# Performance work log

Measured on AMD Instinct MI355X. Metric: run time of the kernel, lower is better.

## Reference

```python
import jax, jax.numpy as jnp
import numpy as np

N_USERS, N_ITEMS, DIM, LAYERS, NNZ = 50000, 50000, 128, 2, 1600000
N = N_USERS + N_ITEMS


def setup_inputs() -> dict:
    key = jax.random.key(0)
    ks = jax.random.split(key, 8)
    adj_row = jax.random.randint(ks[0], (NNZ,), 0, N, dtype=jnp.int32)
    adj_col = jax.random.randint(ks[1], (NNZ,), 0, N, dtype=jnp.int32)
    # normalized-adjacency-like small positive values (~1/avg_degree)
    adj_vals = jax.random.uniform(ks[2], (NNZ,), dtype=jnp.float32) * 0.0625
    emb = jax.random.normal(ks[3], (N, DIM), dtype=jnp.float32) * 0.1  # xavier-ish
    W1_w = jax.random.normal(ks[4], (LAYERS, DIM, DIM), dtype=jnp.float32) * (1.0 / np.sqrt(DIM))
    W1_b = jnp.zeros((LAYERS, DIM), dtype=jnp.float32)
    W2_w = jax.random.normal(ks[5], (LAYERS, DIM, DIM), dtype=jnp.float32) * (1.0 / np.sqrt(DIM))
    W2_b = jnp.zeros((LAYERS, DIM), dtype=jnp.float32)
    return {"adj_row": adj_row, "adj_col": adj_col, "adj_vals": adj_vals,
            "emb": emb, "W1_w": W1_w, "W1_b": W1_b, "W2_w": W2_w, "W2_b": W2_b}


def reference(adj_row, adj_col, adj_vals, emb, W1_w, W1_b, W2_w, W2_b):
    n = emb.shape[0]
    x = emb
    embs = [x]
    for k in range(W1_w.shape[0]):
        # SpMM: side = norm_adj @ x  (COO gather + segment-sum)
        side = jax.ops.segment_sum(adj_vals[:, None] * x[adj_col], adj_row, num_segments=n)
        # two dense transforms (torch Linear: y = x @ W.T + b), fused add + leaky_relu
        x = jax.nn.leaky_relu((side + x) @ W1_w[k].T + W1_b[k]
                              + (side * x) @ W2_w[k].T + W2_b[k],
                              negative_slope=0.01)
        # dropout is identity in eval mode; L2-normalize rows (F.normalize eps=1e-12)
        x = x / jnp.maximum(jnp.linalg.norm(x, axis=1, keepdims=True), 1e-12)
        embs.append(x)
    return jnp.concatenate(embs, axis=1)  # [N, dim*(layers+1)]
```

## Files before the change

### kernel.cpp

```cpp
#include <hip/hip_runtime.h>
#include <stdint.h>

#define N_NODES 100000
#define NPAD    100032
#define DIM 128
#define NNZ_E 1600000
#define SCAN_TILE 2048
#define N_TILES ((N_NODES + SCAN_TILE - 1) / SCAN_TILE)

typedef float f32x4  __attribute__((ext_vector_type(4)));
typedef short bf16x8 __attribute__((ext_vector_type(8)));

union B8 { uint4 q; unsigned u[4]; bf16x8 v; };

__device__ __forceinline__ unsigned short f2bs(float f) {
    unsigned u = __builtin_bit_cast(unsigned, f);
    u = (u + 0x7fffu + ((u >> 16) & 1u)) >> 16;
    return (unsigned short)u;
}
__device__ __forceinline__ unsigned pk2(float a, float b) {
    return (unsigned)f2bs(a) | ((unsigned)f2bs(b) << 16);
}
#define UNPK(u32, flo, fhi) { flo = __builtin_bit_cast(float, (unsigned)((u32) << 16)); \
                              fhi = __builtin_bit_cast(float, (unsigned)((u32) & 0xffff0000u)); }

__global__ __launch_bounds__(256) void copy_emb_kernel(
    const float* __restrict__ emb, float* __restrict__ out,
    unsigned* __restrict__ xbuf)
{
    int tid = blockIdx.x * 256 + threadIdx.x;
    int n = tid >> 5, c = tid & 31;
    float4 v = ((const float4*)emb)[tid];
    *((float4*)(out + (size_t)n * 384) + c) = v;
    ((uint2*)xbuf)[(size_t)n * 32 + c] = make_uint2(pk2(v.x, v.y), pk2(v.z, v.w));
}

__global__ __launch_bounds__(256) void wconv_kernel(
    const float* __restrict__ W1, const float* __restrict__ W2,
    unsigned* __restrict__ w1b, unsigned* __restrict__ w2b)
{
    int tid = blockIdx.x * 256 + threadIdx.x;
    float4 a = ((const float4*)W1)[tid];
    float4 b = ((const float4*)W2)[tid];
    ((uint2*)w1b)[tid] = make_uint2(pk2(a.x, a.y), pk2(a.z, a.w));
    ((uint2*)w2b)[tid] = make_uint2(pk2(b.x, b.y), pk2(b.z, b.w));
}

__global__ __launch_bounds__(256) void hist_kernel(
    const int* __restrict__ rows, int* __restrict__ cnt)
{
    int e = blockIdx.x * 256 + threadIdx.x;
    atomicAdd(&cnt[rows[e]], 1);
}

__global__ __launch_bounds__(256) void scan_pass_a(
    const int* __restrict__ cnt, int* __restrict__ tile_sums)
{
    __shared__ int sdata[256];
    int base = blockIdx.x * SCAN_TILE + threadIdx.x * 8;
    int s = 0;
    #pragma unroll
    for (int q = 0; q < 8; ++q) {
        int i = base + q;
        s += (i < N_NODES) ? cnt[i] : 0;
    }
    sdata[threadIdx.x] = s;
    __syncthreads();
    for (int off = 128; off >= 1; off >>= 1) {
        if (threadIdx.x < off) sdata[threadIdx.x] += sdata[threadIdx.x + off];
        __syncthreads();
    }
    if (threadIdx.x == 0) tile_sums[blockIdx.x] = sdata[0];
}

__global__ void scan_pass_b(int* __restrict__ tile_sums)
{
    if (threadIdx.x == 0 && blockIdx.x == 0) {
        int acc = 0;
        for (int i = 0; i < N_TILES; ++i) {
            int t = tile_sums[i]; tile_sums[i] = acc; acc += t;
        }
    }
}

__global__ __launch_bounds__(256) void scan_pass_c(
    const int* __restrict__ cnt, const int* __restrict__ tile_offs,
    int* __restrict__ row_ptr)
{
    __shared__ int spart[256];
    int t = threadIdx.x;
    int base = blockIdx.x * SCAN_TILE + t * 8;
    int loc[8];
    int s = 0;
    #pragma unroll
    for (int q = 0; q < 8; ++q) {
        int i = base + q;
        int c = (i < N_NODES) ? cnt[i] : 0;
        loc[q] = s; s += c;
    }
    spart[t] = s;
    __syncthreads();
    for (int off = 1; off < 256; off <<= 1) {
        int v = (t >= off) ? spart[t - off] : 0;
        __syncthreads();
        spart[t] += v;
        __syncthreads();
    }
    int exoff = tile_offs[blockIdx.x] + spart[t] - s;
    #pragma unroll
    for (int q = 0; q < 8; ++q) {
        int i = base + q;
        if (i <= N_NODES) row_ptr[i] = exoff + loc[q];
    }
}

__global__ __launch_bounds__(256) void scatter_kernel(
    const int* __restrict__ rows, const int* __restrict__ cols,
    const float* __restrict__ vals, const int* __restrict__ row_ptr,
    int* __restrict__ fill, int2* __restrict__ edges)
{
    int e = blockIdx.x * 256 + threadIdx.x;
    int r = rows[e];
    int pos = row_ptr[r] + atomicAdd(&fill[r], 1);
    edges[pos] = make_int2(cols[e], __float_as_int(vals[e]));
}

__global__ __launch_bounds__(256) void spmm_gather_bf16(
    const int* __restrict__ row_ptr, const int2* __restrict__ edges,
    const unsigned* __restrict__ xb, unsigned* __restrict__ sideb)
{
    int row  = blockIdx.x * 4 + (threadIdx.x >> 6);
    int lane = threadIdx.x & 63;
    int beg = row_ptr[row], end = row_ptr[row + 1];
    float ax = 0.f, ay = 0.f;
    int i = beg;
    for (; i + 3 < end; i += 4) {
        int2 e0 = edges[i], e1 = edges[i + 1], e2 = edges[i + 2], e3 = edges[i + 3];
        unsigned u0 = xb[(size_t)e0.x * 64 + lane];
        unsigned u1 = xb[(size_t)e1.x * 64 + lane];
        unsigned u2 = xb[(size_t)e2.x * 64 + lane];
        unsigned u3 = xb[(size_t)e3.x * 64 + lane];
        float v0 = __int_as_float(e0.y), v1 = __int_as_float(e1.y);
        float v2 = __int_as_float(e2.y), v3 = __int_as_float(e3.y);
        float lo, hi;
        UNPK(u0, lo, hi); ax += v0 * lo; ay += v0 * hi;
        UNPK(u1, lo, hi); ax += v1 * lo; ay += v1 * hi;
        UNPK(u2, lo, hi); ax += v2 * lo; ay += v2 * hi;
        UNPK(u3, lo, hi); ax += v3 * lo; ay += v3 * hi;
    }
    for (; i < end; ++i) {
        int2 e = edges[i];
        unsigned u = xb[(size_t)e.x * 64 + lane];
        float v = __int_as_float(e.y), lo, hi;
        UNPK(u, lo, hi); ax += v * lo; ay += v * hi;
    }
    sideb[(size_t)row * 64 + lane] = pk2(ax, ay);
}

__global__ __launch_bounds__(256) void dense_mfma_kernel(
    const unsigned* __restrict__ sideb, unsigned* __restrict__ xbuf,
    const unsigned* __restrict__ w1b, const unsigned* __restrict__ w2b,
    const float* __restrict__ b1, const float* __restrict__ b2,
    float* __restrict__ out, int outoff, int write_x)
{
    __shared__ float sPart[256];
    const int t = threadIdx.x;
    const int wave = t >> 6, lane = t & 63;
    const int q = lane >> 4, r = lane & 15;
    const int colbase = wave * 32;

    bf16x8 Wf[2][2][4];
    {
        const uint4* w1p = (const uint4*)w1b;
        const uint4* w2p = (const uint4*)w2b;
        #pragma unroll
        for (int nt = 0; nt < 2; ++nt) {
            int j = colbase + nt * 16 + r;
            #pragma unroll
            for (int kk = 0; kk < 4; ++kk) {
                B8 a, b;
                a.q = w1p[j * 16 + kk * 4 + q];
                b.q = w2p[j * 16 + kk * 4 + q];
                Wf[0][nt][kk] = a.v;
                Wf[1][nt][kk] = b.v;
            }
        }
    }
    const float bias0 = b1[colbase + r]      + b2[colbase + r];
    const float bias1 = b1[colbase + 16 + r] + b2[colbase + 16 + r];

    const int base = blockIdx.x * 64;
    f32x4 acc[4][2];
    #pragma unroll
    for (int mt = 0; mt < 4; ++mt) {
        acc[mt][0] = (f32x4){0.f, 0.f, 0.f, 0.f};
        acc[mt][1] = (f32x4){0.f, 0.f, 0.f, 0.f};
    }

    #pragma unroll
    for (int mt = 0; mt < 4; ++mt) {
        const size_t node = (size_t)(base + mt * 16 + r);
        const uint4* sp = (const uint4*)sideb + node * 16 + q;
        const uint4* xp = (const uint4*)xbuf  + node * 16 + q;
        #pragma unroll
        for (int kk = 0; kk < 4; ++kk) {
            uint4 sv = sp[kk * 4];
            uint4 xv = xp[kk * 4];
            float s0,s1,s2,s3,s4,s5,s6,s7;
            float x0,x1,x2,x3,x4,x5,x6,x7;
            UNPK(sv.x, s0, s1); UNPK(sv.y, s2, s3);
            UNPK(sv.z, s4, s5); UNPK(sv.w, s6, s7);
            UNPK(xv.x, x0, x1); UNPK(xv.y, x2, x3);
            UNPK(xv.z, x4, x5); UNPK(xv.w, x6, x7);
            B8 a1, a2;
            a1.u[0] = pk2(s0 + x0, s1 + x1);
            a1.u[1] = pk2(s2 + x2, s3 + x3);
            a1.u[2] = pk2(s4 + x4, s5 + x5);
            a1.u[3] = pk2(s6 + x6, s7 + x7);
            a2.u[0] = pk2(s0 * x0, s1 * x1);
            a2.u[1] = pk2(s2 * x2, s3 * x3);
            a2.u[2] = pk2(s4 * x4, s5 * x5);
            a2.u[3] = pk2(s6 * x6, s7 * x7);
            acc[mt][0] = __builtin_amdgcn_mfma_f32_16x16x32_bf16(a1.v, Wf[0][0][kk], acc[mt][0], 0, 0, 0);
            acc[mt][0] = __builtin_amdgcn_mfma_f32_16x16x32_bf16(a2.v, Wf[1][0][kk], acc[mt][0], 0, 0, 0);
            acc[mt][1] = __builtin_amdgcn_mfma_f32_16x16x32_bf16(a1.v, Wf[0][1][kk], acc[mt][1], 0, 0, 0);
            acc[mt][1] = __builtin_amdgcn_mfma_f32_16x16x32_bf16(a2.v, Wf[1][1][kk], acc[mt][1], 0, 0, 0);
        }
    }

    #pragma unroll
    for (int mt = 0; mt < 4; ++mt) {
        #pragma unroll
        for (int i = 0; i < 4; ++i) {
            float y0 = acc[mt][0][i] + bias0; y0 = (y0 >= 0.f) ? y0 : 0.01f * y0;
            float y1 = acc[mt][1][i] + bias1; y1 = (y1 >= 0.f) ? y1 : 0.01f * y1;
            acc[mt][0][i] = y0; acc[mt][1][i] = y1;
            float s = y0 * y0 + y1 * y1;
            s += __shfl_xor(s, 1); s += __shfl_xor(s, 2);
            s += __shfl_xor(s, 4); s += __shfl_xor(s, 8);
            if (r == 0) sPart[wave * 64 + mt * 16 + q * 4 + i] = s;
        }
    }
    __syncthreads();

    #pragma unroll
    for (int mt = 0; mt < 4; ++mt) {
        #pragma unroll
        for (int i = 0; i < 4; ++i) {
            int nl = mt * 16 + q * 4 + i;
            float tot = sPart[nl] + sPart[64 + nl] + sPart[128 + nl] + sPart[192 + nl];
            float inv = 1.0f / fmaxf(sqrtf(tot), 1e-12f);
            int node = base + nl;
            if (node < N_NODES) {
                float y0 = acc[mt][0][i] * inv;
                float y1 = acc[mt][1][i] * inv;
                out[(size_t)node * 384 + outoff + colbase + r]      = y0;
                out[(size_t)node * 384 + outoff + colbase + 16 + r] = y1;
                if (write_x) {
                    ((unsigned short*)xbuf)[(size_t)node * 128 + colbase + r]      = f2bs(y0);
                    ((unsigned short*)xbuf)[(size_t)node * 128 + colbase + 16 + r] = f2bs(y1);
                }
            }
        }
    }
}

extern "C" void kernel_launch(void* const* d_in, const int* in_sizes, int n_in,
                              void* d_out, int out_size, void* d_ws, size_t ws_size,
                              hipStream_t stream)
{
    const int*   adj_row  = (const int*)d_in[0];
    const int*   adj_col  = (const int*)d_in[1];
    const float* adj_vals = (const float*)d_in[2];
    const float* emb      = (const float*)d_in[3];
    const float* W1_w     = (const float*)d_in[4];
    const float* W1_b     = (const float*)d_in[5];
    const float* W2_w     = (const float*)d_in[6];
    const float* W2_b     = (const float*)d_in[7];
    float* out = (float*)d_out;

    uint8_t* w = (uint8_t*)d_ws;
    unsigned* xbuf    = (unsigned*)(w);
    unsigned* sideb   = (unsigned*)(w + 25608192);
    int2*     edges   = (int2*)    (w + 51216384);
    unsigned* w1b     = (unsigned*)(w + 64016384);
    unsigned* w2b     = (unsigned*)(w + 64081920);
    int*      row_ptr = (int*)     (w + 64147456);
    int*      cnt     = (int*)     (w + 64547472);
    int*      tsums   = (int*)     (w + 64947488);

    wconv_kernel<<<32, 256, 0, stream>>>(W1_w, W2_w, w1b, w2b);
    copy_emb_kernel<<<N_NODES * 32 / 256, 256, 0, stream>>>(emb, out, xbuf);
    hipMemsetAsync(xbuf  + (size_t)N_NODES * 64, 0, (NPAD - N_NODES) * 256, stream);
    hipMemsetAsync(sideb + (size_t)N_NODES * 64, 0, (NPAD - N_NODES) * 256, stream);

    hipMemsetAsync(cnt, 0, (size_t)N_NODES * sizeof(int), stream);
    hist_kernel<<<NNZ_E / 256, 256, 0, stream>>>(adj_row, cnt);
    scan_pass_a<<<N_TILES, 256, 0, stream>>>(cnt, tsums);
    scan_pass_b<<<1, 64, 0, stream>>>(tsums);
    scan_pass_c<<<N_TILES, 256, 0, stream>>>(cnt, tsums, row_ptr);
    hipMemsetAsync(cnt, 0, (size_t)N_NODES * sizeof(int), stream);
    scatter_kernel<<<NNZ_E / 256, 256, 0, stream>>>(
        adj_row, adj_col, adj_vals, row_ptr, cnt, edges);

    for (int k = 0; k < 2; ++k) {
        spmm_gather_bf16<<<N_NODES / 4, 256, 0, stream>>>(row_ptr, edges, xbuf, sideb);
        dense_mfma_kernel<<<NPAD / 64, 256, 0, stream>>>(
            sideb, xbuf, w1b + k * 8192, w2b + k * 8192,
            W1_b + k * DIM, W2_b + k * DIM,
            out, DIM * (k + 1), (k == 0) ? 1 : 0);
    }
}
```

Baseline: 631.9 us.

## Fuse memsets into kernels, pipeline SpMM edge loads, stage dense inputs in LDS

Replaces the hipMemsetAsync calls by zeroing inside the prep, copy and gather kernels, and drops the second cnt memset by decrementing cnt during the scatter. Uses the hardware v_cvt_pk_bf16_f32 instruction for bf16 packing, parallelises scan_pass_b with wave shuffles, and software-pipelines edge loads in the SpMM in groups of eight. The dense kernel now builds (side+x) and (side*x) cooperatively into swizzled LDS before the MFMA loop. Each of these trims launch count or latency, but the LDS staging adds a barrier and shared-memory use that can reduce occupancy.

```diff
diff --git a/kernel.cpp b/kernel.cpp
--- a/kernel.cpp
+++ b/kernel.cpp
@@ -18,8 +18,10 @@
     u = (u + 0x7fffu + ((u >> 16) & 1u)) >> 16;
     return (unsigned short)u;
 }
-__device__ __forceinline__ unsigned pk2(float a, float b) {
-    return (unsigned)f2bs(a) | ((unsigned)f2bs(b) << 16);
+__device__ __forceinline__ unsigned cvtpk(float lo, float hi) {
+    unsigned r;
+    asm("v_cvt_pk_bf16_f32 %0, %1, %2" : "=v"(r) : "v"(lo), "v"(hi));
+    return r;
 }
 #define UNPK(u32, flo, fhi) { flo = __builtin_bit_cast(float, (unsigned)((u32) << 16)); \
                               fhi = __builtin_bit_cast(float, (unsigned)((u32) & 0xffff0000u)); }
@@ -30,20 +32,28 @@
 {
     int tid = blockIdx.x * 256 + threadIdx.x;
     int n = tid >> 5, c = tid & 31;
-    float4 v = ((const float4*)emb)[tid];
-    *((float4*)(out + (size_t)n * 384) + c) = v;
-    ((uint2*)xbuf)[(size_t)n * 32 + c] = make_uint2(pk2(v.x, v.y), pk2(v.z, v.w));
-}
-
-__global__ __launch_bounds__(256) void wconv_kernel(
+    if (n < N_NODES) {
+        float4 v = ((const float4*)emb)[tid];
+        *((float4*)(out + (size_t)n * 384) + c) = v;
+        ((uint2*)xbuf)[(size_t)n * 32 + c] = make_uint2(cvtpk(v.x, v.y), cvtpk(v.z, v.w));
+    } else {
+        ((uint2*)xbuf)[(size_t)n * 32 + c] = make_uint2(0u, 0u);
+    }
+}
+
+__global__ __launch_bounds__(256) void prep_kernel(
     const float* __restrict__ W1, const float* __restrict__ W2,
-    unsigned* __restrict__ w1b, unsigned* __restrict__ w2b)
+    unsigned* __restrict__ w1b, unsigned* __restrict__ w2b,
+    int* __restrict__ cnt)
 {
     int tid = blockIdx.x * 256 + threadIdx.x;
-    float4 a = ((const float4*)W1)[tid];
-    float4 b = ((const float4*)W2)[tid];
-    ((uint2*)w1b)[tid] = make_uint2(pk2(a.x, a.y), pk2(a.z, a.w));
-    ((uint2*)w2b)[tid] = make_uint2(pk2(b.x, b.y), pk2(b.z, b.w));
+    if (tid < 8192) {
+        float4 a = ((const float4*)W1)[tid];
+        float4 b = ((const float4*)W2)[tid];
+        ((uint2*)w1b)[tid] = make_uint2(cvtpk(a.x, a.y), cvtpk(a.z, a.w));
+        ((uint2*)w2b)[tid] = make_uint2(cvtpk(b.x, b.y), cvtpk(b.z, b.w));
+    }
+    if (tid < 25000) ((uint4*)cnt)[tid] = make_uint4(0u, 0u, 0u, 0u);
 }
 
 __global__ __launch_bounds__(256) void hist_kernel(
@@ -75,12 +85,16 @@
 
 __global__ void scan_pass_b(int* __restrict__ tile_sums)
 {
-    if (threadIdx.x == 0 && blockIdx.x == 0) {
-        int acc = 0;
-        for (int i = 0; i < N_TILES; ++i) {
-            int t = tile_sums[i]; tile_sums[i] = acc; acc += t;
-        }
-    }
+    int lane = threadIdx.x;
+    int v = (lane < N_TILES) ? tile_sums[lane] : 0;
+    #pragma unroll
+    for (int off = 1; off < 64; off <<= 1) {
+        int u = __shfl_up(v, off);
+        if (lane >= off) v += u;
+    }
+    int ex = __shfl_up(v, 1);
+    if (lane == 0) ex = 0;
+    if (lane < N_TILES) tile_sums[lane] = ex;
 }
 
 __global__ __launch_bounds__(256) void scan_pass_c(
@@ -117,11 +131,11 @@
 __global__ __launch_bounds__(256) void scatter_kernel(
     const int* __restrict__ rows, const int* __restrict__ cols,
     const float* __restrict__ vals, const int* __restrict__ row_ptr,
-    int* __restrict__ fill, int2* __restrict__ edges)
+    int* __restrict__ cnt, int2* __restrict__ edges)
 {
     int e = blockIdx.x * 256 + threadIdx.x;
     int r = rows[e];
-    int pos = row_ptr[r] + atomicAdd(&fill[r], 1);
+    int pos = row_ptr[r] + atomicSub(&cnt[r], 1) - 1;
     edges[pos] = make_int2(cols[e], __float_as_int(vals[e]));
 }
 
@@ -131,30 +145,47 @@
 {
     int row  = blockIdx.x * 4 + (threadIdx.x >> 6);
     int lane = threadIdx.x & 63;
+    if (row >= N_NODES) {
+        sideb[(size_t)row * 64 + lane] = 0u;
+        return;
+    }
     int beg = row_ptr[row], end = row_ptr[row + 1];
     float ax = 0.f, ay = 0.f;
     int i = beg;
-    for (; i + 3 < end; i += 4) {
-        int2 e0 = edges[i], e1 = edges[i + 1], e2 = edges[i + 2], e3 = edges[i + 3];
-        unsigned u0 = xb[(size_t)e0.x * 64 + lane];
-        unsigned u1 = xb[(size_t)e1.x * 64 + lane];
-        unsigned u2 = xb[(size_t)e2.x * 64 + lane];
-        unsigned u3 = xb[(size_t)e3.x * 64 + lane];
-        float v0 = __int_as_float(e0.y), v1 = __int_as_float(e1.y);
-        float v2 = __int_as_float(e2.y), v3 = __int_as_float(e3.y);
-        float lo, hi;
-        UNPK(u0, lo, hi); ax += v0 * lo; ay += v0 * hi;
-        UNPK(u1, lo, hi); ax += v1 * lo; ay += v1 * hi;
-        UNPK(u2, lo, hi); ax += v2 * lo; ay += v2 * hi;
-        UNPK(u3, lo, hi); ax += v3 * lo; ay += v3 * hi;
+    int nfull = (end - beg) & ~7;
+    if (nfull) {
+        int2 e[8];
+        #pragma unroll
+        for (int u = 0; u < 8; ++u) e[u] = edges[i + u];
+        for (int g = 8; g < nfull; g += 8) {
+            int2 f[8];
+            #pragma unroll
+            for (int u = 0; u < 8; ++u) f[u] = edges[i + 8 + u];
+            #pragma unroll
+            for (int u = 0; u < 8; ++u) {
+                unsigned xu = xb[(size_t)e[u].x * 64 + lane];
+                float v = __int_as_float(e[u].y), lo, hi;
+                UNPK(xu, lo, hi); ax += v * lo; ay += v * hi;
+            }
+            #pragma unroll
+            for (int u = 0; u < 8; ++u) e[u] = f[u];
+            i += 8;
+        }
+        #pragma unroll
+        for (int u = 0; u < 8; ++u) {
+            unsigned xu = xb[(size_t)e[u].x * 64 + lane];
+            float v = __int_as_float(e[u].y), lo, hi;
+            UNPK(xu, lo, hi); ax += v * lo; ay += v * hi;
+        }
+        i += 8;
     }
     for (; i < end; ++i) {
         int2 e = edges[i];
-        unsigned u = xb[(size_t)e.x * 64 + lane];
+        unsigned xu = xb[(size_t)e.x * 64 + lane];
         float v = __int_as_float(e.y), lo, hi;
-        UNPK(u, lo, hi); ax += v * lo; ay += v * hi;
-    }
-    sideb[(size_t)row * 64 + lane] = pk2(ax, ay);
+        UNPK(xu, lo, hi); ax += v * lo; ay += v * hi;
+    }
+    sideb[(size_t)row * 64 + lane] = cvtpk(ax, ay);
 }
 
 __global__ __launch_bounds__(256) void dense_mfma_kernel(
@@ -163,11 +194,15 @@
     const float* __restrict__ b1, const float* __restrict__ b2,
     float* __restrict__ out, int outoff, int write_x)
 {
+    __shared__ __align__(16) unsigned sA1[64 * 64];
+    __shared__ __align__(16) unsigned sA2[64 * 64];
     __shared__ float sPart[256];
+
     const int t = threadIdx.x;
     const int wave = t >> 6, lane = t & 63;
     const int q = lane >> 4, r = lane & 15;
     const int colbase = wave * 32;
+    const int base = blockIdx.x * 64;
 
     bf16x8 Wf[2][2][4];
     {
@@ -189,38 +224,60 @@
     const float bias0 = b1[colbase + r]      + b2[colbase + r];
     const float bias1 = b1[colbase + 16 + r] + b2[colbase + 16 + r];
 
-    const int base = blockIdx.x * 64;
-    f32x4 acc[4][2];
-    #pragma unroll
-    for (int mt = 0; mt < 4; ++mt) {
-        acc[mt][0] = (f32x4){0.f, 0.f, 0.f, 0.f};
-        acc[mt][1] = (f32x4){0.f, 0.f, 0.f, 0.f};
-    }
-
-    #pragma unroll
-    for (int mt = 0; mt < 4; ++mt) {
-        const size_t node = (size_t)(base + mt * 16 + r);
-        const uint4* sp = (const uint4*)sideb + node * 16 + q;
-        const uint4* xp = (const uint4*)xbuf  + node * 16 + q;
-        #pragma unroll
-        for (int kk = 0; kk < 4; ++kk) {
-            uint4 sv = sp[kk * 4];
-            uint4 xv = xp[kk * 4];
+    {
+        const int n = t >> 2, seg = t & 3;
+        const uint4* sp = (const uint4*)sideb + ((size_t)(base + n)) * 16 + seg * 4;
+        const uint4* xp = (const uint4*)xbuf  + ((size_t)(base + n)) * 16 + seg * 4;
+        unsigned* d1 = sA1 + n * 64;
+        unsigned* d2 = sA2 + n * 64;
+        const int sw = n & 7, seg4 = seg * 4;
+        #pragma unroll
+        for (int j = 0; j < 4; ++j) {
+            uint4 sv = sp[j];
+            uint4 xv = xp[j];
             float s0,s1,s2,s3,s4,s5,s6,s7;
             float x0,x1,x2,x3,x4,x5,x6,x7;
             UNPK(sv.x, s0, s1); UNPK(sv.y, s2, s3);
             UNPK(sv.z, s4, s5); UNPK(sv.w, s6, s7);
             UNPK(xv.x, x0, x1); UNPK(xv.y, x2, x3);
             UNPK(xv.z, x4, x5); UNPK(xv.w, x6, x7);
+            uint4 a1q, a2q;
+            a1q.x = cvtpk(s0 + x0, s1 + x1);
+            a1q.y = cvtpk(s2 + x2, s3 + x3);
+            a1q.z = cvtpk(s4 + x4, s5 + x5);
+            a1q.w = cvtpk(s6 + x6, s7 + x7);
+            a2q.x = cvtpk(s0 * x0, s1 * x1);
+            a2q.y = cvtpk(s2 * x2, s3 * x3);
+            a2q.z = cvtpk(s4 * x4, s5 * x5);
+            a2q.w = cvtpk(s6 * x6, s7 * x7);
+            int slot = (seg4 + j) ^ sw;
+            *(uint4*)(d1 + slot * 4) = a1q;
+            *(uint4*)(d2 + slot * 4) = a2q;
+        }
+    }
+    __syncthreads();
+
+    f32x4 acc[4][2];
+    #pragma unroll
+    for (int mt = 0; mt < 4; ++mt) {
+        acc[mt][0] = (f32x4){0.f, 0.f, 0.f, 0.f};
+        acc[mt][1] = (f32x4){0.f, 0.f, 0.f, 0.f};
+    }
+    int slotk[4];
+    {
+        const int sw = r & 7;
+        #pragma unroll
+        for (int kk = 0; kk < 4; ++kk) slotk[kk] = ((kk * 4 + q) ^ sw) * 4;
+    }
+    #pragma unroll
+    for (int mt = 0; mt < 4; ++mt) {
+        const unsigned* p1 = sA1 + (mt * 16 + r) * 64;
+        const unsigned* p2 = sA2 + (mt * 16 + r) * 64;
+        #pragma unroll
+        for (int kk = 0; kk < 4; ++kk) {
             B8 a1, a2;
-            a1.u[0] = pk2(s0 + x0, s1 + x1);
-            a1.u[1] = pk2(s2 + x2, s3 + x3);
-            a1.u[2] = pk2(s4 + x4, s5 + x5);
-            a1.u[3] = pk2(s6 + x6, s7 + x7);
-            a2.u[0] = pk2(s0 * x0, s1 * x1);
-            a2.u[1] = pk2(s2 * x2, s3 * x3);
-            a2.u[2] = pk2(s4 * x4, s5 * x5);
-            a2.u[3] = pk2(s6 * x6, s7 * x7);
+            a1.q = *(const uint4*)(p1 + slotk[kk]);
+            a2.q = *(const uint4*)(p2 + slotk[kk]);
             acc[mt][0] = __builtin_amdgcn_mfma_f32_16x16x32_bf16(a1.v, Wf[0][0][kk], acc[mt][0], 0, 0, 0);
             acc[mt][0] = __builtin_amdgcn_mfma_f32_16x16x32_bf16(a2.v, Wf[1][0][kk], acc[mt][0], 0, 0, 0);
             acc[mt][1] = __builtin_amdgcn_mfma_f32_16x16x32_bf16(a1.v, Wf[0][1][kk], acc[mt][1], 0, 0, 0);
@@ -289,22 +346,18 @@
     int*      cnt     = (int*)     (w + 64547472);
     int*      tsums   = (int*)     (w + 64947488);
 
-    wconv_kernel<<<32, 256, 0, stream>>>(W1_w, W2_w, w1b, w2b);
-    copy_emb_kernel<<<N_NODES * 32 / 256, 256, 0, stream>>>(emb, out, xbuf);
-    hipMemsetAsync(xbuf  + (size_t)N_NODES * 64, 0, (NPAD - N_NODES) * 256, stream);
-    hipMemsetAsync(sideb + (size_t)N_NODES * 64, 0, (NPAD - N_NODES) * 256, stream);
-
-    hipMemsetAsync(cnt, 0, (size_t)N_NODES * sizeof(int), stream);
+    prep_kernel<<<128, 256, 0, stream>>>(W1_w, W2_w, w1b, w2b, cnt);
+    copy_emb_kernel<<<NPAD * 32 / 256, 256, 0, stream>>>(emb, out, xbuf);
+
     hist_kernel<<<NNZ_E / 256, 256, 0, stream>>>(adj_row, cnt);
     scan_pass_a<<<N_TILES, 256, 0, stream>>>(cnt, tsums);
     scan_pass_b<<<1, 64, 0, stream>>>(tsums);
     scan_pass_c<<<N_TILES, 256, 0, stream>>>(cnt, tsums, row_ptr);
-    hipMemsetAsync(cnt, 0, (size_t)N_NODES * sizeof(int), stream);
     scatter_kernel<<<NNZ_E / 256, 256, 0, stream>>>(
         adj_row, adj_col, adj_vals, row_ptr, cnt, edges);
 
     for (int k = 0; k < 2; ++k) {
-        spmm_gather_bf16<<<N_NODES / 4, 256, 0, stream>>>(row_ptr, edges, xbuf, sideb);
+        spmm_gather_bf16<<<NPAD / 4, 256, 0, stream>>>(row_ptr, edges, xbuf, sideb);
         dense_mfma_kernel<<<NPAD / 64, 256, 0, stream>>>(
             sideb, xbuf, w1b + k * 8192, w2b + k * 8192,
             W1_b + k * DIM, W2_b + k * DIM,
```

Measured after the change: 577.6 us. 1.09x faster.
